# Performance work log

Hardware: AMD Instinct MI355X
Metric: run time of the kernel (lower is better)

Reference implementation:

```python
import jax, jax.numpy as jnp
import numpy as np

N_INTERVALS = 40          # control intervals (240 = 6 * n)
DT = 0.25                 # interval_duration
CAR_WIDTH = 2.0
N_OBST = 3                # (13 - 4) / 3
BATCH = 131072


def _dynamics(state, u, t):
    # state: (..., 4) = [px, py, theta, v]; u: (..., 2) = [accel, omega]
    px, py, th, v = state[..., 0], state[..., 1], state[..., 2], state[..., 3]
    a, w = u[..., 0], u[..., 1]
    return jnp.stack([px + v * jnp.cos(th) * t,
                      py + v * jnp.sin(th) * t,
                      th + w * t,
                      v + a * t], axis=-1)


def setup_inputs() -> dict:
    key = jax.random.key(0)
    k1, k2, k3 = jax.random.split(key, 3)
    predictions = jax.random.normal(k1, (BATCH, 240), dtype=jnp.float32)
    targets = jax.random.normal(k2, (BATCH, 240), dtype=jnp.float32)
    inputs = jax.random.normal(k3, (BATCH, 13), dtype=jnp.float32)
    return {"predictions": predictions, "targets": targets, "inputs": inputs}


def reference(predictions, targets, inputs):
    n, t = N_INTERVALS, DT
    B = predictions.shape[0]

    mse = jnp.mean((predictions - targets) ** 2)

    x = predictions[:, : 4 * n].reshape(B, n, 4)          # states per interval
    u = predictions[:, 4 * n: 6 * n].reshape(B, n, 2)     # controls per interval
    x0 = inputs[:, :4]                                    # (B, 4)
    obstacles = inputs[:, 4:].reshape(B, N_OBST, 3)       # (B, 3, 3) = [ox, oy, r]

    # dynamics_error accumulates the per-interval residuals, then a single norm
    prev = jnp.concatenate([x0[:, None, :], x[:, :-1, :]], axis=1)  # (B, n, 4)
    dyn_resid = jnp.sum(x - _dynamics(prev, u, t), axis=1)          # (B, 4)
    dyn_err = jnp.linalg.norm(dyn_resid, axis=-1)                   # (B,)

    # obstacle term: sum over obstacles and states of dist - (r + car_width)^2
    dx = x[:, None, :, 0] - obstacles[:, :, None, 0]                # (B, 3, n)
    dy = x[:, None, :, 1] - obstacles[:, :, None, 1]
    dist = jnp.sqrt(dx * dx + dy * dy)
    rad2 = (obstacles[:, :, 2] + CAR_WIDTH) ** 2                    # (B, 3)
    obst_err = jnp.sum(dist - rad2[:, :, None], axis=(1, 2))        # (B,)

    constraint = jnp.mean(dyn_err + obst_err)
    return mse + constraint
```

## Files before the change

kernel.cpp:

```cpp
#include <hip/hip_runtime.h>


#define NTHREADS 256

__global__ void zero_ws_kernel(float* ws) {
    ws[0] = 0.0f;
    ws[1] = 0.0f;
}

__global__ __launch_bounds__(NTHREADS) void constraint_main_kernel(
    const float* __restrict__ pred,
    const float* __restrict__ targ,
    const float* __restrict__ inp,
    float* __restrict__ ws,
    int B)
{
    const float DT = 0.25f;
    int row = blockIdx.x * NTHREADS + threadIdx.x;

    float mse = 0.0f;
    float cons = 0.0f;

    if (row < B) {
        const float4* p4 = reinterpret_cast<const float4*>(pred + (size_t)row * 240);
        const float4* t4 = reinterpret_cast<const float4*>(targ + (size_t)row * 240);
        const float*  in = inp + (size_t)row * 13;

        float x0px = in[0], x0py = in[1], x0th = in[2], x0v = in[3];
        float ox0 = in[4],  oy0 = in[5];
        float ox1 = in[7],  oy1 = in[8];
        float ox2 = in[10], oy2 = in[11];
        float r0_ = in[6]  + 2.0f;
        float r1_ = in[9]  + 2.0f;
        float r2_ = in[12] + 2.0f;
        float rad2sum = r0_ * r0_ + r1_ * r1_ + r2_ * r2_;

        float cv = 0.0f, sv = 0.0f;
        float sum_dist = 0.0f;
        float prev_th = x0th, prev_v = x0v;
        float4 xl = make_float4(0.f, 0.f, 0.f, 0.f);

        #pragma unroll 4
        for (int k = 0; k < 40; ++k) {
            float4 pv = p4[k];
            float4 tv = t4[k];
            float d0 = pv.x - tv.x, d1 = pv.y - tv.y;
            float d2 = pv.z - tv.z, d3 = pv.w - tv.w;
            mse += d0 * d0 + d1 * d1 + d2 * d2 + d3 * d3;

            float s, c;
            __sincosf(prev_th, &s, &c);
            cv += prev_v * c;
            sv += prev_v * s;

            float dx, dy;
            dx = pv.x - ox0; dy = pv.y - oy0; sum_dist += sqrtf(dx * dx + dy * dy);
            dx = pv.x - ox1; dy = pv.y - oy1; sum_dist += sqrtf(dx * dx + dy * dy);
            dx = pv.x - ox2; dy = pv.y - oy2; sum_dist += sqrtf(dx * dx + dy * dy);

            prev_th = pv.z;
            prev_v  = pv.w;
            xl = pv;
        }

        float sum_a = 0.0f, sum_w = 0.0f;
        #pragma unroll 4
        for (int m = 0; m < 20; ++m) {
            float4 pv = p4[40 + m];
            float4 tv = t4[40 + m];
            float d0 = pv.x - tv.x, d1 = pv.y - tv.y;
            float d2 = pv.z - tv.z, d3 = pv.w - tv.w;
            mse += d0 * d0 + d1 * d1 + d2 * d2 + d3 * d3;
            sum_a += pv.x + pv.z;
            sum_w += pv.y + pv.w;
        }

        float rr0 = xl.x - x0px - DT * cv;
        float rr1 = xl.y - x0py - DT * sv;
        float rr2 = xl.z - x0th - DT * sum_w;
        float rr3 = xl.w - x0v  - DT * sum_a;
        float dyn_err = sqrtf(rr0 * rr0 + rr1 * rr1 + rr2 * rr2 + rr3 * rr3);
        float obst_err = sum_dist - 40.0f * rad2sum;
        cons = dyn_err + obst_err;
    }

    #pragma unroll
    for (int off = 32; off > 0; off >>= 1) {
        mse  += __shfl_down(mse,  off);
        cons += __shfl_down(cons, off);
    }

    __shared__ float smse[NTHREADS / 64];
    __shared__ float scons[NTHREADS / 64];
    int wid  = threadIdx.x >> 6;
    int lane = threadIdx.x & 63;
    if (lane == 0) { smse[wid] = mse; scons[wid] = cons; }
    __syncthreads();
    if (threadIdx.x == 0) {
        float m = smse[0] + smse[1] + smse[2] + smse[3];
        float c = scons[0] + scons[1] + scons[2] + scons[3];
        atomicAdd(&ws[0], m);
        atomicAdd(&ws[1], c);
    }
}

__global__ void finalize_kernel(const float* __restrict__ ws, float* __restrict__ out, int B) {
    float nb = (float)B;
    out[0] = ws[0] / (nb * 240.0f) + ws[1] / nb;
}

extern "C" void kernel_launch(void* const* d_in, const int* in_sizes, int n_in,
                              void* d_out, int out_size, void* d_ws, size_t ws_size,
                              hipStream_t stream) {
    const float* pred = (const float*)d_in[0];
    const float* targ = (const float*)d_in[1];
    const float* inp  = (const float*)d_in[2];
    float* out = (float*)d_out;
    float* ws  = (float*)d_ws;

    int B = in_sizes[0] / 240;

    zero_ws_kernel<<<1, 1, 0, stream>>>(ws);
    int grid = (B + NTHREADS - 1) / NTHREADS;
    constraint_main_kernel<<<grid, NTHREADS, 0, stream>>>(pred, targ, inp, ws, B);
    finalize_kernel<<<1, 1, 0, stream>>>(ws, out, B);
}
```

Baseline: 285.5 us.

## Split each row across four threads and replace atomics with per-block partials

Each row is now handled by four cooperating lanes that interleave float4 loads, with shuffle reductions combining their partial sums and the last state. The sincos recurrence is reindexed so each lane handles its own states, and the initial state term is added once. Per-row inputs are staged in shared memory. The global atomic accumulation and zero kernel are replaced by per-block partial outputs reduced in a parallel finalize kernel. This aims to improve memory access coalescing and parallelism, at the cost of extra shuffles and shared-memory staging.

```diff
diff --git a/kernel.cpp b/kernel.cpp
--- a/kernel.cpp
+++ b/kernel.cpp
@@ -2,72 +2,78 @@
 
 
 #define NTHREADS 256
-
-__global__ void zero_ws_kernel(float* ws) {
-    ws[0] = 0.0f;
-    ws[1] = 0.0f;
-}
+#define ROWS_PER_BLOCK 64
 
 __global__ __launch_bounds__(NTHREADS) void constraint_main_kernel(
     const float* __restrict__ pred,
     const float* __restrict__ targ,
     const float* __restrict__ inp,
-    float* __restrict__ ws,
+    float* __restrict__ partial,
     int B)
 {
     const float DT = 0.25f;
-    int row = blockIdx.x * NTHREADS + threadIdx.x;
+    const int tid  = threadIdx.x;
+    const int sub  = tid & 3;
+    const int rloc = tid >> 2;
+    const int row  = blockIdx.x * ROWS_PER_BLOCK + rloc;
 
-    float mse = 0.0f;
-    float cons = 0.0f;
+    __shared__ float sinp[ROWS_PER_BLOCK * 13];
+    {
+        const int base = blockIdx.x * ROWS_PER_BLOCK * 13;
+        const int tot  = ROWS_PER_BLOCK * 13;
+        const int avail = B * 13 - base;
+        for (int idx = tid; idx < tot; idx += NTHREADS) {
+            float v = 0.0f;
+            if (idx < avail) v = inp[base + idx];
+            sinp[idx] = v;
+        }
+    }
+    __syncthreads();
+
+    float mse = 0.0f, cons = 0.0f;
 
     if (row < B) {
         const float4* p4 = reinterpret_cast<const float4*>(pred + (size_t)row * 240);
         const float4* t4 = reinterpret_cast<const float4*>(targ + (size_t)row * 240);
-        const float*  in = inp + (size_t)row * 13;
+        const float*  in = &sinp[rloc * 13];
 
-        float x0px = in[0], x0py = in[1], x0th = in[2], x0v = in[3];
-        float ox0 = in[4],  oy0 = in[5];
-        float ox1 = in[7],  oy1 = in[8];
-        float ox2 = in[10], oy2 = in[11];
-        float r0_ = in[6]  + 2.0f;
-        float r1_ = in[9]  + 2.0f;
-        float r2_ = in[12] + 2.0f;
-        float rad2sum = r0_ * r0_ + r1_ * r1_ + r2_ * r2_;
+        const float ox0 = in[4],  oy0 = in[5];
+        const float ox1 = in[7],  oy1 = in[8];
+        const float ox2 = in[10], oy2 = in[11];
 
-        float cv = 0.0f, sv = 0.0f;
-        float sum_dist = 0.0f;
-        float prev_th = x0th, prev_v = x0v;
-        float4 xl = make_float4(0.f, 0.f, 0.f, 0.f);
+        float cv = 0.0f, sv = 0.0f, sum_dist = 0.0f;
+        float sum_a = 0.0f, sum_w = 0.0f;
+        float xlx = 0.0f, xly = 0.0f, xlth = 0.0f, xlv = 0.0f;
 
-        #pragma unroll 4
-        for (int k = 0; k < 40; ++k) {
+        #pragma unroll
+        for (int i = 0; i < 10; ++i) {
+            const int k = sub + 4 * i;
             float4 pv = p4[k];
             float4 tv = t4[k];
             float d0 = pv.x - tv.x, d1 = pv.y - tv.y;
             float d2 = pv.z - tv.z, d3 = pv.w - tv.w;
             mse += d0 * d0 + d1 * d1 + d2 * d2 + d3 * d3;
 
-            float s, c;
-            __sincosf(prev_th, &s, &c);
-            cv += prev_v * c;
-            sv += prev_v * s;
+            if (k != 39) {
+                float s, c;
+                __sincosf(pv.z, &s, &c);
+                cv += pv.w * c;
+                sv += pv.w * s;
+            } else {
+                xlx = pv.x; xly = pv.y; xlth = pv.z; xlv = pv.w;
+            }
 
             float dx, dy;
             dx = pv.x - ox0; dy = pv.y - oy0; sum_dist += sqrtf(dx * dx + dy * dy);
             dx = pv.x - ox1; dy = pv.y - oy1; sum_dist += sqrtf(dx * dx + dy * dy);
             dx = pv.x - ox2; dy = pv.y - oy2; sum_dist += sqrtf(dx * dx + dy * dy);
-
-            prev_th = pv.z;
-            prev_v  = pv.w;
-            xl = pv;
         }
 
-        float sum_a = 0.0f, sum_w = 0.0f;
-        #pragma unroll 4
-        for (int m = 0; m < 20; ++m) {
-            float4 pv = p4[40 + m];
-            float4 tv = t4[40 + m];
+        #pragma unroll
+        for (int i = 0; i < 5; ++i) {
+            const int m = 40 + sub + 4 * i;
+            float4 pv = p4[m];
+            float4 tv = t4[m];
             float d0 = pv.x - tv.x, d1 = pv.y - tv.y;
             float d2 = pv.z - tv.z, d3 = pv.w - tv.w;
             mse += d0 * d0 + d1 * d1 + d2 * d2 + d3 * d3;
@@ -75,13 +81,40 @@
             sum_w += pv.y + pv.w;
         }
 
-        float rr0 = xl.x - x0px - DT * cv;
-        float rr1 = xl.y - x0py - DT * sv;
-        float rr2 = xl.z - x0th - DT * sum_w;
-        float rr3 = xl.w - x0v  - DT * sum_a;
-        float dyn_err = sqrtf(rr0 * rr0 + rr1 * rr1 + rr2 * rr2 + rr3 * rr3);
-        float obst_err = sum_dist - 40.0f * rad2sum;
-        cons = dyn_err + obst_err;
+        #pragma unroll
+        for (int m = 1; m < 4; m <<= 1) {
+            cv       += __shfl_xor(cv, m);
+            sv       += __shfl_xor(sv, m);
+            sum_a    += __shfl_xor(sum_a, m);
+            sum_w    += __shfl_xor(sum_w, m);
+            sum_dist += __shfl_xor(sum_dist, m);
+        }
+
+        const int lane = tid & 63;
+        const int src  = lane | 3;
+        xlx  = __shfl(xlx,  src);
+        xly  = __shfl(xly,  src);
+        xlth = __shfl(xlth, src);
+        xlv  = __shfl(xlv,  src);
+
+        if (sub == 0) {
+            const float x0px = in[0], x0py = in[1], x0th = in[2], x0v = in[3];
+            const float r0 = in[6]  + 2.0f;
+            const float r1 = in[9]  + 2.0f;
+            const float r2 = in[12] + 2.0f;
+            float s, c;
+            __sincosf(x0th, &s, &c);
+            cv += x0v * c;
+            sv += x0v * s;
+
+            float rr0 = xlx  - x0px - DT * cv;
+            float rr1 = xly  - x0py - DT * sv;
+            float rr2 = xlth - x0th - DT * sum_w;
+            float rr3 = xlv  - x0v  - DT * sum_a;
+            float dyn_err = sqrtf(rr0 * rr0 + rr1 * rr1 + rr2 * rr2 + rr3 * rr3);
+            float rad2sum = r0 * r0 + r1 * r1 + r2 * r2;
+            cons = dyn_err + sum_dist - 40.0f * rad2sum;
+        }
     }
 
     #pragma unroll
@@ -92,21 +125,43 @@
 
     __shared__ float smse[NTHREADS / 64];
     __shared__ float scons[NTHREADS / 64];
-    int wid  = threadIdx.x >> 6;
-    int lane = threadIdx.x & 63;
+    const int wid  = threadIdx.x >> 6;
+    const int lane = threadIdx.x & 63;
     if (lane == 0) { smse[wid] = mse; scons[wid] = cons; }
     __syncthreads();
     if (threadIdx.x == 0) {
         float m = smse[0] + smse[1] + smse[2] + smse[3];
         float c = scons[0] + scons[1] + scons[2] + scons[3];
-        atomicAdd(&ws[0], m);
-        atomicAdd(&ws[1], c);
+        partial[2 * blockIdx.x]     = m;
+        partial[2 * blockIdx.x + 1] = c;
     }
 }
 
-__global__ void finalize_kernel(const float* __restrict__ ws, float* __restrict__ out, int B) {
-    float nb = (float)B;
-    out[0] = ws[0] / (nb * 240.0f) + ws[1] / nb;
+__global__ __launch_bounds__(256) void finalize_kernel(
+    const float* __restrict__ partial, float* __restrict__ out,
+    int nblocks, int B)
+{
+    float m = 0.0f, c = 0.0f;
+    for (int i = threadIdx.x; i < nblocks; i += 256) {
+        m += partial[2 * i];
+        c += partial[2 * i + 1];
+    }
+    #pragma unroll
+    for (int off = 32; off > 0; off >>= 1) {
+        m += __shfl_down(m, off);
+        c += __shfl_down(c, off);
+    }
+    __shared__ float sm[4], sc[4];
+    const int wid  = threadIdx.x >> 6;
+    const int lane = threadIdx.x & 63;
+    if (lane == 0) { sm[wid] = m; sc[wid] = c; }
+    __syncthreads();
+    if (threadIdx.x == 0) {
+        float mm = sm[0] + sm[1] + sm[2] + sm[3];
+        float cc = sc[0] + sc[1] + sc[2] + sc[3];
+        float nb = (float)B;
+        out[0] = mm / (nb * 240.0f) + cc / nb;
+    }
 }
 
 extern "C" void kernel_launch(void* const* d_in, const int* in_sizes, int n_in,
@@ -118,10 +173,9 @@
     float* out = (float*)d_out;
     float* ws  = (float*)d_ws;
 
-    int B = in_sizes[0] / 240;
+    const int B = in_sizes[0] / 240;
+    const int grid = (B + ROWS_PER_BLOCK - 1) / ROWS_PER_BLOCK;
 
-    zero_ws_kernel<<<1, 1, 0, stream>>>(ws);
-    int grid = (B + NTHREADS - 1) / NTHREADS;
     constraint_main_kernel<<<grid, NTHREADS, 0, stream>>>(pred, targ, inp, ws, B);
-    finalize_kernel<<<1, 1, 0, stream>>>(ws, out, B);
+    finalize_kernel<<<1, 256, 0, stream>>>(ws, out, grid, B);
 }
```

New measurement: 270.2 us. -5.3%, faster.
